# Optimization experiments

Measured on AMD Instinct MI355X. Metric: run time of the kernel, lower is better.

Reference implementation:

```python
import jax, jax.numpy as jnp
import numpy as np

B, N, DOP, DM, H = 8, 2048, 256, 256, 256  # batch, n_ops==n_machines, dims


def setup_inputs() -> dict:
    key = jax.random.key(0)
    ks = jax.random.split(key, 21)
    s = 0.02
    inp = {
        "operation_features": jax.random.normal(ks[0], (B, N, DOP), jnp.float32),
        "machine_features": jax.random.normal(ks[1], (B, N, DM), jnp.float32),
        "type_match_mask": jax.random.bernoulli(ks[2], 0.3, (B, N, N)).astype(jnp.float32),
        "same_type_mask": jax.random.bernoulli(ks[3], 0.3, (B, N, N)).astype(jnp.float32),
        "oma_q_w": jax.random.normal(ks[4], (H, DM), jnp.float32) * s,
        "oma_q_b": jnp.zeros((H,), jnp.float32),
        "oma_kv_w": jax.random.normal(ks[5], (2 * H, DOP), jnp.float32) * s,
        "oma_kv_b": jnp.zeros((2 * H,), jnp.float32),
        "oma_s_w": jax.random.normal(ks[6], (1, 2 * H), jnp.float32) * s,
        "oma_s_b": jnp.zeros((1,), jnp.float32),
        "oma_o_w": jax.random.normal(ks[7], (DM, H), jnp.float32) * s,
        "oma_o_b": jnp.zeros((DM,), jnp.float32),
        "sa_w_w": jax.random.normal(ks[8], (3 * H, DM), jnp.float32) * s,
        "sa_w_b": jnp.zeros((3 * H,), jnp.float32),
        "sa_s_w": jax.random.normal(ks[9], (1, 2 * H), jnp.float32) * s,
        "sa_s_b": jnp.zeros((1,), jnp.float32),
        "sa_o_w": jax.random.normal(ks[10], (DM, H), jnp.float32) * s,
        "sa_o_b": jnp.zeros((DM,), jnp.float32),
        "mix_w": jax.random.normal(ks[11], (DM, 2 * DM), jnp.float32) * s,
        "mix_b": jnp.zeros((DM,), jnp.float32),
    }
    return inp


def reference(operation_features, machine_features, type_match_mask, same_type_mask,
              oma_q_w, oma_q_b, oma_kv_w, oma_kv_b, oma_s_w, oma_s_b, oma_o_w, oma_o_b,
              sa_w_w, sa_w_b, sa_s_w, sa_s_b, sa_o_w, sa_o_b, mix_w, mix_b):
    # --- OperationMachineAttention ---
    q = machine_features @ oma_q_w.T + oma_q_b            # (B,M,H)
    kv = operation_features @ oma_kv_w.T + oma_kv_b       # (B,C,2H)
    k, v = jnp.split(kv, 2, axis=-1)
    # Linear(cat([q,k])) == q @ W[:, :H].T + k @ W[:, H:].T + b (additive-score factorization)
    sq = jnp.einsum('bmh,h->bm', q, oma_s_w[0, :H])
    sk = jnp.einsum('bch,h->bc', k, oma_s_w[0, H:])
    scores = jax.nn.leaky_relu(sq[:, :, None] + sk[:, None, :] + oma_s_b[0])  # (B,M,C)
    p = jax.nn.softmax(scores * type_match_mask, axis=-1)
    wf = jnp.einsum('bmc,bch->bmh', p, v)
    operation_machine = wf @ oma_o_w.T + oma_o_b           # (B,M,DM)

    # --- SelfAttention over machines ---
    w3 = machine_features @ sa_w_w.T + sa_w_b              # (B,C,3H)
    q2, k2, v2 = jnp.split(w3, 3, axis=-1)
    sq2 = jnp.einsum('bih,h->bi', q2, sa_s_w[0, :H])
    sk2 = jnp.einsum('bjh,h->bj', k2, sa_s_w[0, H:])
    s2 = jax.nn.leaky_relu(sq2[:, :, None] + sk2[:, None, :] + sa_s_b[0])  # (B,C,C)
    p2 = jax.nn.softmax(s2 * same_type_mask, axis=-1)
    machine_machine = jnp.einsum('bij,bjh->bih', p2, v2) @ sa_o_w.T + sa_o_b  # (B,C,DM)

    # --- mix ---
    mixed = jnp.concatenate([operation_machine, machine_machine], axis=-1)
    return mixed @ mix_w.T + mix_b                          # (B,N,DM)
```

## Files before the change

kernel.cpp:

```cpp
#include <hip/hip_runtime.h>
#include <stdint.h>
#include <stddef.h>

#define B_ 8
#define N_ 2048
#define C_ 2048
#define D_ 256
#define H_ 256

typedef __bf16 bf16x8 __attribute__((ext_vector_type(8)));
typedef __bf16 bf16x4 __attribute__((ext_vector_type(4)));
typedef float f32x4 __attribute__((ext_vector_type(4)));

#define MFMA16(a, b, c) __builtin_amdgcn_mfma_f32_16x16x32_bf16((a), (b), (c), 0, 0, 0)

__global__ __launch_bounds__(256) void k0_vectors(
    const float* __restrict__ oma_q_w, const float* __restrict__ oma_q_b,
    const float* __restrict__ oma_kv_w, const float* __restrict__ oma_kv_b,
    const float* __restrict__ oma_s_w, const float* __restrict__ oma_s_b,
    const float* __restrict__ sa_w_w, const float* __restrict__ sa_w_b,
    const float* __restrict__ sa_s_w, const float* __restrict__ sa_s_b,
    float* __restrict__ wq_v, float* __restrict__ wk_v,
    float* __restrict__ wq2_v, float* __restrict__ wk2_v,
    float* __restrict__ sb)
{
    int d = threadIdx.x;
    float a0 = 0.f, a1 = 0.f, a2 = 0.f, a3 = 0.f;
    for (int h = 0; h < 256; ++h) {
        a0 += oma_q_w[h * 256 + d] * oma_s_w[h];
        a1 += oma_kv_w[h * 256 + d] * oma_s_w[256 + h];
        a2 += sa_w_w[h * 256 + d] * sa_s_w[h];
        a3 += sa_w_w[(256 + h) * 256 + d] * sa_s_w[256 + h];
    }
    wq_v[d] = a0; wk_v[d] = a1; wq2_v[d] = a2; wk2_v[d] = a3;

    int h = d;
    float p1 = oma_q_b[h] * oma_s_w[h] + oma_kv_b[h] * oma_s_w[256 + h];
    float p2 = sa_w_b[h] * sa_s_w[h] + sa_w_b[256 + h] * sa_s_w[256 + h];
    for (int o = 32; o; o >>= 1) { p1 += __shfl_xor(p1, o); p2 += __shfl_xor(p2, o); }
    __shared__ float redA[4], redB[4];
    int wv = threadIdx.x >> 6;
    if ((threadIdx.x & 63) == 0) { redA[wv] = p1; redB[wv] = p2; }
    __syncthreads();
    if (threadIdx.x == 0) {
        sb[0] = redA[0] + redA[1] + redA[2] + redA[3] + oma_s_b[0];
        sb[1] = redB[0] + redB[1] + redB[2] + redB[3] + sa_s_b[0];
    }
}

__global__ __launch_bounds__(256) void k1_wcat(
    const float* __restrict__ mix_w, const float* __restrict__ mix_b,
    const float* __restrict__ oma_o_w, const float* __restrict__ oma_o_b,
    const float* __restrict__ sa_o_w, const float* __restrict__ sa_o_b,
    __bf16* __restrict__ Wcat, float* __restrict__ b_total)
{
    int d = blockIdx.x, h = threadIdx.x;
    const float* mwr = mix_w + d * 512;
    float w1 = 0.f, w2 = 0.f;
    for (int e = 0; e < 256; ++e) {
        w1 += mwr[e] * oma_o_w[e * 256 + h];
        w2 += mwr[256 + e] * sa_o_w[e * 256 + h];
    }
    Wcat[d * 512 + h] = (__bf16)w1;
    Wcat[d * 512 + 256 + h] = (__bf16)w2;

    float pb = mwr[h] * oma_o_b[h] + mwr[256 + h] * sa_o_b[h];
    for (int o = 32; o; o >>= 1) pb += __shfl_xor(pb, o);
    __shared__ float red[4];
    if ((h & 63) == 0) red[h >> 6] = pb;
    __syncthreads();
    if (h == 0) b_total[d] = mix_b[d] + red[0] + red[1] + red[2] + red[3];
}

__global__ __launch_bounds__(256) void k2_scores(
    const float* __restrict__ op, const float* __restrict__ mach,
    const float* __restrict__ wq_v, const float* __restrict__ wk_v,
    const float* __restrict__ wq2_v, const float* __restrict__ wk2_v,
    const float* __restrict__ sb,
    float* __restrict__ sqp, float* __restrict__ skv,
    float* __restrict__ sq2p, float* __restrict__ sk2v)
{
    int t = threadIdx.x, lane = t & 63, wv = t >> 6;
    size_t n = (size_t)blockIdx.x * 4 + wv;
    const float4 mf = *(const float4*)(mach + n * 256 + lane * 4);
    const float4 of = *(const float4*)(op + n * 256 + lane * 4);
    const float4 q4 = *(const float4*)(wq_v + lane * 4);
    const float4 k4 = *(const float4*)(wk_v + lane * 4);
    const float4 q24 = *(const float4*)(wq2_v + lane * 4);
    const float4 k24 = *(const float4*)(wk2_v + lane * 4);
    float s1 = mf.x * q4.x + mf.y * q4.y + mf.z * q4.z + mf.w * q4.w;
    float s2 = of.x * k4.x + of.y * k4.y + of.z * k4.z + of.w * k4.w;
    float s3 = mf.x * q24.x + mf.y * q24.y + mf.z * q24.z + mf.w * q24.w;
    float s4 = mf.x * k24.x + mf.y * k24.y + mf.z * k24.z + mf.w * k24.w;
    for (int o = 32; o; o >>= 1) {
        s1 += __shfl_xor(s1, o); s2 += __shfl_xor(s2, o);
        s3 += __shfl_xor(s3, o); s4 += __shfl_xor(s4, o);
    }
    if (lane == 0) {
        sqp[n] = s1 + sb[0]; skv[n] = s2;
        sq2p[n] = s3 + sb[1]; sk2v[n] = s4;
    }
}

__global__ __launch_bounds__(256, 2) void k3_vgemm(
    const float* __restrict__ op, const float* __restrict__ mach,
    const float* __restrict__ oma_kv_w, const float* __restrict__ sa_w_w,
    __bf16* __restrict__ vt)
{
    __shared__ __attribute__((aligned(16))) __bf16 As[64][72];
    __shared__ __attribute__((aligned(16))) __bf16 Bs[64][72];
    int t = threadIdx.x;
    int bid = blockIdx.x;
    int which = bid >> 10;
    int r = bid & 1023;
    int b = r >> 7;
    int ht = (r >> 5) & 3;
    int ct = r & 31;

    const float* Aglob = (which ? (sa_w_w + 512 * 256) : (oma_kv_w + 256 * 256)) + ht * 64 * 256;
    const float* Bglob = (which ? mach : op) + ((size_t)b * N_ + ct * 64) * 256;

    int lane = t & 63, wv = t >> 6;
    int l15 = lane & 15, qo = (lane >> 4) * 8;
    int rr = t >> 4;
    int dd = (t & 15) * 4;

    f32x4 acc[4] = {};

    for (int d0 = 0; d0 < 256; d0 += 64) {
        #pragma unroll
        for (int p = 0; p < 4; ++p) {
            float4 av = *(const float4*)(Aglob + (size_t)(p * 16 + rr) * 256 + d0 + dd);
            float4 bv = *(const float4*)(Bglob + (size_t)(p * 16 + rr) * 256 + d0 + dd);
            bf16x4 a4, b4;
            a4[0] = (__bf16)av.x; a4[1] = (__bf16)av.y; a4[2] = (__bf16)av.z; a4[3] = (__bf16)av.w;
            b4[0] = (__bf16)bv.x; b4[1] = (__bf16)bv.y; b4[2] = (__bf16)bv.z; b4[3] = (__bf16)bv.w;
            *(bf16x4*)&As[p * 16 + rr][dd] = a4;
            *(bf16x4*)&Bs[p * 16 + rr][dd] = b4;
        }
        __syncthreads();
        #pragma unroll
        for (int kb = 0; kb < 2; ++kb) {
            bf16x8 bfr = *(const bf16x8*)&Bs[16 * wv + l15][kb * 32 + qo];
            #pragma unroll
            for (int rt = 0; rt < 4; ++rt) {
                bf16x8 afr = *(const bf16x8*)&As[16 * rt + l15][kb * 32 + qo];
                acc[rt] = MFMA16(afr, bfr, acc[rt]);
            }
        }
        __syncthreads();
    }
    #pragma unroll
    for (int rt = 0; rt < 4; ++rt)
        #pragma unroll
        for (int j = 0; j < 4; ++j)
            As[16 * rt + (lane >> 4) * 4 + j][16 * wv + l15] = (__bf16)acc[rt][j];
    __syncthreads();
    int hh = t >> 2, cb = (t & 3) * 16;
    __bf16* orow = vt + (((size_t)(which * 8 + b)) * 256 + ht * 64 + hh) * 2048 + ct * 64 + cb;
    *(bf16x8*)(orow) = *(const bf16x8*)&As[hh][cb];
    *(bf16x8*)(orow + 8) = *(const bf16x8*)&As[hh][cb + 8];
}

__global__ __launch_bounds__(256, 2) void k4_attn(
    const float* __restrict__ tmask, const float* __restrict__ smask,
    const float* __restrict__ sqp, const float* __restrict__ skv,
    const float* __restrict__ sq2p, const float* __restrict__ sk2v,
    const __bf16* __restrict__ vt,
    __bf16* __restrict__ wfcat)
{
    __shared__ __attribute__((aligned(16))) __bf16 eA[64][72];
    __shared__ __attribute__((aligned(16))) __bf16 vB[256][72];
    __shared__ float rowsum[64];

    int t = threadIdx.x;
    int bid = blockIdx.x;
    int which = bid >> 8;
    int r = bid & 255;
    int b = r >> 5;
    int m0 = (r & 31) * 64;

    const float* mask = (which ? smask : tmask) + ((size_t)b * N_ + m0) * C_;
    const float* sqrow = (which ? sq2p : sqp) + b * N_ + m0;
    const float* skrow = (which ? sk2v : skv) + b * N_;
    const __bf16* vbase = vt + ((size_t)(which * 8 + b)) * 256 * 2048;

    int lane = t & 63, wv = t >> 6;
    int l15 = lane & 15, qo = (lane >> 4) * 8;
    int mrow = t >> 2;
    int cqb = (t & 3) * 16;
    int vh = t >> 3;
    int vc = (t & 7) * 8;

    float sqv = sqrow[mrow];
    float psum = 0.f;
    f32x4 acc[4][4] = {};

    bf16x8 vv[8];
    float mk[16], skc[16];

    auto load_tiles = [&](int c0) {
        #pragma unroll
        for (int p = 0; p < 8; ++p)
            vv[p] = *(const bf16x8*)(vbase + (size_t)(p * 32 + vh) * 2048 + c0 + vc);
        #pragma unroll
        for (int i = 0; i < 4; ++i) {
            float4 m4 = *(const float4*)(mask + (size_t)mrow * C_ + c0 + cqb + i * 4);
            float4 s4 = *(const float4*)(skrow + c0 + cqb + i * 4);
            mk[4 * i + 0] = m4.x; mk[4 * i + 1] = m4.y; mk[4 * i + 2] = m4.z; mk[4 * i + 3] = m4.w;
            skc[4 * i + 0] = s4.x; skc[4 * i + 1] = s4.y; skc[4 * i + 2] = s4.z; skc[4 * i + 3] = s4.w;
        }
    };
    load_tiles(0);

    for (int c0 = 0; c0 < C_; c0 += 64) {
        #pragma unroll
        for (int p = 0; p < 8; ++p)
            *(bf16x8*)&vB[p * 32 + vh][vc] = vv[p];
        bf16x8 e0, e1;
        #pragma unroll
        for (int i = 0; i < 16; ++i) {
            float s = sqv + skc[i];
            s = s > 0.f ? s : 0.01f * s;
            float e = __expf(s * mk[i]);
            psum += e;
            if (i < 8) e0[i] = (__bf16)e; else e1[i - 8] = (__bf16)e;
        }
        *(bf16x8*)&eA[mrow][cqb] = e0;
        *(bf16x8*)&eA[mrow][cqb + 8] = e1;
        __syncthreads();
        int cn = c0 + 64; if (cn >= C_) cn = 0;
        load_tiles(cn);
        #pragma unroll
        for (int kb = 0; kb < 2; ++kb) {
            bf16x8 afr[4];
            #pragma unroll
            for (int rt = 0; rt < 4; ++rt)
                afr[rt] = *(const bf16x8*)&eA[16 * rt + l15][kb * 32 + qo];
            #pragma unroll
            for (int ctile = 0; ctile < 4; ++ctile) {
                bf16x8 bfr = *(const bf16x8*)&vB[64 * wv + 16 * ctile + l15][kb * 32 + qo];
                #pragma unroll
                for (int rt = 0; rt < 4; ++rt)
                    acc[rt][ctile] = MFMA16(afr[rt], bfr, acc[rt][ctile]);
            }
        }
        __syncthreads();
    }

    float rs = psum;
    rs += __shfl_xor(rs, 1);
    rs += __shfl_xor(rs, 2);
    if ((t & 3) == 0) rowsum[mrow] = rs;
    __syncthreads();

    __bf16* obuf = &vB[0][0];
    #pragma unroll
    for (int rt = 0; rt < 4; ++rt) {
        #pragma unroll
        for (int j = 0; j < 4; ++j) {
            int m = 16 * rt + (lane >> 4) * 4 + j;
            float inv = __builtin_amdgcn_rcpf(rowsum[m]);
            #pragma unroll
            for (int ctile = 0; ctile < 4; ++ctile)
                obuf[m * 264 + 64 * wv + 16 * ctile + l15] = (__bf16)(acc[rt][ctile][j] * inv);
        }
    }
    __syncthreads();
    int m = t >> 2, cb = (t & 3) * 64;
    __bf16* wrow = wfcat + ((size_t)(b * N_ + m0 + m)) * 512 + which * 256 + cb;
    #pragma unroll
    for (int k = 0; k < 8; ++k)
        *(bf16x8*)(wrow + k * 8) = *(const bf16x8*)&obuf[m * 264 + cb + k * 8];
}

__global__ __launch_bounds__(256, 2) void k5_out(
    const __bf16* __restrict__ wfcat, const __bf16* __restrict__ Wcat,
    const float* __restrict__ b_total, float* __restrict__ out)
{
    __shared__ __attribute__((aligned(16))) __bf16 As[64][72];
    __shared__ __attribute__((aligned(16))) __bf16 Bs[256][72];
    __shared__ float bias[256];
    int t = threadIdx.x;
    int n0 = blockIdx.x * 64;
    int lane = t & 63, wv = t >> 6, l15 = lane & 15, qo = (lane >> 4) * 8;
    bias[t] = b_total[t];
    int ar = t >> 3;
    int ac = (t & 7) * 8;
    f32x4 acc[4][4] = {};

    for (int k0 = 0; k0 < 512; k0 += 64) {
        #pragma unroll
        for (int p = 0; p < 2; ++p)
            *(bf16x8*)&As[p * 32 + ar][ac] =
                *(const bf16x8*)(wfcat + (size_t)(n0 + p * 32 + ar) * 512 + k0 + ac);
        #pragma unroll
        for (int p = 0; p < 8; ++p)
            *(bf16x8*)&Bs[p * 32 + ar][ac] =
                *(const bf16x8*)(Wcat + (size_t)(p * 32 + ar) * 512 + k0 + ac);
        __syncthreads();
        #pragma unroll
        for (int kb = 0; kb < 2; ++kb) {
            bf16x8 afr[4];
            #pragma unroll
            for (int rt = 0; rt < 4; ++rt)
                afr[rt] = *(const bf16x8*)&As[16 * rt + l15][kb * 32 + qo];
            #pragma unroll
            for (int ct = 0; ct < 4; ++ct) {
                bf16x8 bfr = *(const bf16x8*)&Bs[64 * wv + 16 * ct + l15][kb * 32 + qo];
                #pragma unroll
                for (int rt = 0; rt < 4; ++rt)
                    acc[rt][ct] = MFMA16(afr[rt], bfr, acc[rt][ct]);
            }
        }
        __syncthreads();
    }
    #pragma unroll
    for (int rt = 0; rt < 4; ++rt) {
        #pragma unroll
        for (int ct = 0; ct < 4; ++ct) {
            int d = 64 * wv + 16 * ct + l15;
            float bv = bias[d];
            #pragma unroll
            for (int j = 0; j < 4; ++j) {
                int m = 16 * rt + (lane >> 4) * 4 + j;
                out[(size_t)(n0 + m) * 256 + d] = acc[rt][ct][j] + bv;
            }
        }
    }
}

extern "C" void kernel_launch(void* const* d_in, const int* in_sizes, int n_in,
                              void* d_out, int out_size, void* d_ws, size_t ws_size,
                              hipStream_t stream)
{
    const float* op_feat  = (const float*)d_in[0];
    const float* mach_feat= (const float*)d_in[1];
    const float* tmask    = (const float*)d_in[2];
    const float* smask    = (const float*)d_in[3];
    const float* oma_q_w  = (const float*)d_in[4];
    const float* oma_q_b  = (const float*)d_in[5];
    const float* oma_kv_w = (const float*)d_in[6];
    const float* oma_kv_b = (const float*)d_in[7];
    const float* oma_s_w  = (const float*)d_in[8];
    const float* oma_s_b  = (const float*)d_in[9];
    const float* oma_o_w  = (const float*)d_in[10];
    const float* oma_o_b  = (const float*)d_in[11];
    const float* sa_w_w   = (const float*)d_in[12];
    const float* sa_w_b   = (const float*)d_in[13];
    const float* sa_s_w   = (const float*)d_in[14];
    const float* sa_s_b   = (const float*)d_in[15];
    const float* sa_o_w   = (const float*)d_in[16];
    const float* sa_o_b   = (const float*)d_in[17];
    const float* mix_w    = (const float*)d_in[18];
    const float* mix_b    = (const float*)d_in[19];

    char* ws = (char*)d_ws;
    float* wq_v   = (float*)(ws + 0);
    float* wk_v   = (float*)(ws + 1024);
    float* wq2_v  = (float*)(ws + 2048);
    float* wk2_v  = (float*)(ws + 3072);
    float* sb     = (float*)(ws + 4096);
    float* btot   = (float*)(ws + 4352);
    float* sqp    = (float*)(ws + 8192);
    float* skv    = (float*)(ws + 73728);
    float* sq2p   = (float*)(ws + 139264);
    float* sk2v   = (float*)(ws + 204800);
    __bf16* Wcat  = (__bf16*)(ws + 270336);
    __bf16* vt    = (__bf16*)(ws + 532480);
    __bf16* wfcat = (__bf16*)(ws + 17309696);
    float* outp   = (float*)d_out;

    k0_vectors<<<1, 256, 0, stream>>>(oma_q_w, oma_q_b, oma_kv_w, oma_kv_b,
                                      oma_s_w, oma_s_b, sa_w_w, sa_w_b,
                                      sa_s_w, sa_s_b, wq_v, wk_v, wq2_v, wk2_v, sb);
    k1_wcat<<<256, 256, 0, stream>>>(mix_w, mix_b, oma_o_w, oma_o_b,
                                     sa_o_w, sa_o_b, Wcat, btot);
    k2_scores<<<4096, 256, 0, stream>>>(op_feat, mach_feat, wq_v, wk_v, wq2_v, wk2_v,
                                        sb, sqp, skv, sq2p, sk2v);
    k3_vgemm<<<2048, 256, 0, stream>>>(op_feat, mach_feat, oma_kv_w, sa_w_w, vt);
    k4_attn<<<512, 256, 0, stream>>>(tmask, smask, sqp, skv, sq2p, sk2v, vt, wfcat);
    k5_out<<<256, 256, 0, stream>>>(wfcat, Wcat, btot, outp);
}
```

Baseline: 453.1 us.

## Restructure V-projection GEMM and shrink attention row tiles with swizzled LDS

Measured after the change: 560.7 us. +23.8%, slower.

```diff
diff --git a/kernel.cpp b/kernel.cpp
--- a/kernel.cpp
+++ b/kernel.cpp
@@ -107,41 +107,47 @@
     const float* __restrict__ oma_kv_w, const float* __restrict__ sa_w_w,
     __bf16* __restrict__ vt)
 {
-    __shared__ __attribute__((aligned(16))) __bf16 As[64][72];
-    __shared__ __attribute__((aligned(16))) __bf16 Bs[64][72];
+    __shared__ __attribute__((aligned(16))) __bf16 Xs[64][264];
+    __shared__ __attribute__((aligned(16))) __bf16 As[64][264];
     int t = threadIdx.x;
     int bid = blockIdx.x;
-    int which = bid >> 10;
-    int r = bid & 1023;
-    int b = r >> 7;
-    int ht = (r >> 5) & 3;
+    int which = bid >> 8;
+    int r = bid & 255;
+    int b = r >> 5;
     int ct = r & 31;
 
-    const float* Aglob = (which ? (sa_w_w + 512 * 256) : (oma_kv_w + 256 * 256)) + ht * 64 * 256;
-    const float* Bglob = (which ? mach : op) + ((size_t)b * N_ + ct * 64) * 256;
+    const float* Wbase = which ? (sa_w_w + 512 * 256) : (oma_kv_w + 256 * 256);
+    const float* Xglob = (which ? mach : op) + ((size_t)b * N_ + ct * 64) * 256;
 
     int lane = t & 63, wv = t >> 6;
     int l15 = lane & 15, qo = (lane >> 4) * 8;
-    int rr = t >> 4;
-    int dd = (t & 15) * 4;
-
-    f32x4 acc[4] = {};
-
-    for (int d0 = 0; d0 < 256; d0 += 64) {
-        #pragma unroll
-        for (int p = 0; p < 4; ++p) {
-            float4 av = *(const float4*)(Aglob + (size_t)(p * 16 + rr) * 256 + d0 + dd);
-            float4 bv = *(const float4*)(Bglob + (size_t)(p * 16 + rr) * 256 + d0 + dd);
-            bf16x4 a4, b4;
+
+    #pragma unroll
+    for (int p = 0; p < 16; ++p) {
+        int row = p * 4 + wv;
+        float4 xv = *(const float4*)(Xglob + (size_t)row * 256 + lane * 4);
+        bf16x4 x4;
+        x4[0] = (__bf16)xv.x; x4[1] = (__bf16)xv.y; x4[2] = (__bf16)xv.z; x4[3] = (__bf16)xv.w;
+        *(bf16x4*)&Xs[row][lane * 4] = x4;
+    }
+
+    for (int ht = 0; ht < 4; ++ht) {
+        __syncthreads();
+        const float* Ag = Wbase + (size_t)ht * 64 * 256;
+        #pragma unroll
+        for (int p = 0; p < 16; ++p) {
+            int row = p * 4 + wv;
+            float4 av = *(const float4*)(Ag + (size_t)row * 256 + lane * 4);
+            bf16x4 a4;
             a4[0] = (__bf16)av.x; a4[1] = (__bf16)av.y; a4[2] = (__bf16)av.z; a4[3] = (__bf16)av.w;
-            b4[0] = (__bf16)bv.x; b4[1] = (__bf16)bv.y; b4[2] = (__bf16)bv.z; b4[3] = (__bf16)bv.w;
-            *(bf16x4*)&As[p * 16 + rr][dd] = a4;
-            *(bf16x4*)&Bs[p * 16 + rr][dd] = b4;
-        }
-        __syncthreads();
-        #pragma unroll
-        for (int kb = 0; kb < 2; ++kb) {
-            bf16x8 bfr = *(const bf16x8*)&Bs[16 * wv + l15][kb * 32 + qo];
+            *(bf16x4*)&As[row][lane * 4] = a4;
+        }
+        __syncthreads();
+
+        f32x4 acc[4] = {};
+        #pragma unroll
+        for (int kb = 0; kb < 8; ++kb) {
+            bf16x8 bfr = *(const bf16x8*)&Xs[16 * wv + l15][kb * 32 + qo];
             #pragma unroll
             for (int rt = 0; rt < 4; ++rt) {
                 bf16x8 afr = *(const bf16x8*)&As[16 * rt + l15][kb * 32 + qo];
@@ -149,36 +155,37 @@
             }
         }
         __syncthreads();
-    }
-    #pragma unroll
-    for (int rt = 0; rt < 4; ++rt)
-        #pragma unroll
-        for (int j = 0; j < 4; ++j)
-            As[16 * rt + (lane >> 4) * 4 + j][16 * wv + l15] = (__bf16)acc[rt][j];
-    __syncthreads();
-    int hh = t >> 2, cb = (t & 3) * 16;
-    __bf16* orow = vt + (((size_t)(which * 8 + b)) * 256 + ht * 64 + hh) * 2048 + ct * 64 + cb;
-    *(bf16x8*)(orow) = *(const bf16x8*)&As[hh][cb];
-    *(bf16x8*)(orow + 8) = *(const bf16x8*)&As[hh][cb + 8];
-}
-
-__global__ __launch_bounds__(256, 2) void k4_attn(
+
+        #pragma unroll
+        for (int rt = 0; rt < 4; ++rt)
+            #pragma unroll
+            for (int j = 0; j < 4; ++j)
+                As[16 * rt + (lane >> 4) * 4 + j][16 * wv + l15] = (__bf16)acc[rt][j];
+        __syncthreads();
+
+        int hh = t >> 2, cb = (t & 3) * 16;
+        __bf16* orow = vt + (((size_t)(which * 8 + b)) * 256 + ht * 64 + hh) * 2048 + ct * 64 + cb;
+        *(bf16x8*)(orow) = *(const bf16x8*)&As[hh][cb];
+        *(bf16x8*)(orow + 8) = *(const bf16x8*)&As[hh][cb + 8];
+    }
+}
+
+__global__ __launch_bounds__(256, 4) void k4_attn(
     const float* __restrict__ tmask, const float* __restrict__ smask,
     const float* __restrict__ sqp, const float* __restrict__ skv,
     const float* __restrict__ sq2p, const float* __restrict__ sk2v,
     const __bf16* __restrict__ vt,
     __bf16* __restrict__ wfcat)
 {
-    __shared__ __attribute__((aligned(16))) __bf16 eA[64][72];
+    __shared__ __attribute__((aligned(16))) __bf16 eA[32][64];
     __shared__ __attribute__((aligned(16))) __bf16 vB[256][72];
-    __shared__ float rowsum[64];
 
     int t = threadIdx.x;
     int bid = blockIdx.x;
-    int which = bid >> 8;
-    int r = bid & 255;
-    int b = r >> 5;
-    int m0 = (r & 31) * 64;
+    int which = bid >> 9;
+    int r = bid & 511;
+    int b = r >> 6;
+    int m0 = (r & 63) * 32;
 
     const float* mask = (which ? smask : tmask) + ((size_t)b * N_ + m0) * C_;
     const float* sqrow = (which ? sq2p : sqp) + b * N_ + m0;
@@ -187,76 +194,85 @@
 
     int lane = t & 63, wv = t >> 6;
     int l15 = lane & 15, qo = (lane >> 4) * 8;
-    int mrow = t >> 2;
-    int cqb = (t & 3) * 16;
+    int mrow = t >> 3;
+    int cc = t & 7;
     int vh = t >> 3;
     int vc = (t & 7) * 8;
 
     float sqv = sqrow[mrow];
     float psum = 0.f;
-    f32x4 acc[4][4] = {};
+    f32x4 acc[2][4] = {};
 
     bf16x8 vv[8];
-    float mk[16], skc[16];
-
-    auto load_tiles = [&](int c0) {
+    float mk[2][8], skc[2][8];
+
+    auto load_mask = [&](int c0, int s) {
+        #pragma unroll
+        for (int i = 0; i < 2; ++i) {
+            float4 m4 = *(const float4*)(mask + (size_t)mrow * C_ + c0 + cc * 8 + i * 4);
+            float4 s4 = *(const float4*)(skrow + c0 + cc * 8 + i * 4);
+            mk[s][4 * i + 0] = m4.x; mk[s][4 * i + 1] = m4.y;
+            mk[s][4 * i + 2] = m4.z; mk[s][4 * i + 3] = m4.w;
+            skc[s][4 * i + 0] = s4.x; skc[s][4 * i + 1] = s4.y;
+            skc[s][4 * i + 2] = s4.z; skc[s][4 * i + 3] = s4.w;
+        }
+    };
+    auto load_v = [&](int c0) {
         #pragma unroll
         for (int p = 0; p < 8; ++p)
             vv[p] = *(const bf16x8*)(vbase + (size_t)(p * 32 + vh) * 2048 + c0 + vc);
-        #pragma unroll
-        for (int i = 0; i < 4; ++i) {
-            float4 m4 = *(const float4*)(mask + (size_t)mrow * C_ + c0 + cqb + i * 4);
-            float4 s4 = *(const float4*)(skrow + c0 + cqb + i * 4);
-            mk[4 * i + 0] = m4.x; mk[4 * i + 1] = m4.y; mk[4 * i + 2] = m4.z; mk[4 * i + 3] = m4.w;
-            skc[4 * i + 0] = s4.x; skc[4 * i + 1] = s4.y; skc[4 * i + 2] = s4.z; skc[4 * i + 3] = s4.w;
-        }
     };
-    load_tiles(0);
+
+    load_mask(0, 0);
+    load_v(0);
+    load_mask(64, 1);
 
     for (int c0 = 0; c0 < C_; c0 += 64) {
+        int s = (c0 >> 6) & 1;
         #pragma unroll
         for (int p = 0; p < 8; ++p)
             *(bf16x8*)&vB[p * 32 + vh][vc] = vv[p];
-        bf16x8 e0, e1;
-        #pragma unroll
-        for (int i = 0; i < 16; ++i) {
-            float s = sqv + skc[i];
-            s = s > 0.f ? s : 0.01f * s;
-            float e = __expf(s * mk[i]);
+        bf16x8 e0;
+        #pragma unroll
+        for (int i = 0; i < 8; ++i) {
+            float sc = sqv + skc[s][i];
+            sc = sc > 0.f ? sc : 0.01f * sc;
+            float e = __expf(sc * mk[s][i]);
             psum += e;
-            if (i < 8) e0[i] = (__bf16)e; else e1[i - 8] = (__bf16)e;
-        }
-        *(bf16x8*)&eA[mrow][cqb] = e0;
-        *(bf16x8*)&eA[mrow][cqb + 8] = e1;
-        __syncthreads();
-        int cn = c0 + 64; if (cn >= C_) cn = 0;
-        load_tiles(cn);
+            e0[i] = (__bf16)e;
+        }
+        *(bf16x8*)&eA[mrow][(cc ^ (mrow & 7)) * 8] = e0;
+        __syncthreads();
+        load_v((c0 + 64) & 2047);
+        load_mask((c0 + 128) & 2047, s);
         #pragma unroll
         for (int kb = 0; kb < 2; ++kb) {
-            bf16x8 afr[4];
-            #pragma unroll
-            for (int rt = 0; rt < 4; ++rt)
-                afr[rt] = *(const bf16x8*)&eA[16 * rt + l15][kb * 32 + qo];
+            bf16x8 afr[2];
+            #pragma unroll
+            for (int rt = 0; rt < 2; ++rt)
+                afr[rt] = *(const bf16x8*)&eA[16 * rt + l15][((kb * 4 + (lane >> 4)) ^ (l15 & 7)) * 8];
             #pragma unroll
             for (int ctile = 0; ctile < 4; ++ctile) {
                 bf16x8 bfr = *(const bf16x8*)&vB[64 * wv + 16 * ctile + l15][kb * 32 + qo];
                 #pragma unroll
-                for (int rt = 0; rt < 4; ++rt)
+                for (int rt = 0; rt < 2; ++rt)
                     acc[rt][ctile] = MFMA16(afr[rt], bfr, acc[rt][ctile]);
             }
         }
         __syncthreads();
     }
 
+    float* rowsum = (float*)(&vB[0][0] + 9000);
     float rs = psum;
     rs += __shfl_xor(rs, 1);
     rs += __shfl_xor(rs, 2);
-    if ((t & 3) == 0) rowsum[mrow] = rs;
+    rs += __shfl_xor(rs, 4);
+    if ((t & 7) == 0) rowsum[mrow] = rs;
     __syncthreads();
 
     __bf16* obuf = &vB[0][0];
     #pragma unroll
-    for (int rt = 0; rt < 4; ++rt) {
+    for (int rt = 0; rt < 2; ++rt) {
         #pragma unroll
         for (int j = 0; j < 4; ++j) {
             int m = 16 * rt + (lane >> 4) * 4 + j;
@@ -267,10 +283,10 @@
         }
     }
     __syncthreads();
-    int m = t >> 2, cb = (t & 3) * 64;
+    int m = t >> 3, cb = (t & 7) * 32;
     __bf16* wrow = wfcat + ((size_t)(b * N_ + m0 + m)) * 512 + which * 256 + cb;
     #pragma unroll
-    for (int k = 0; k < 8; ++k)
+    for (int k = 0; k < 4; ++k)
         *(bf16x8*)(wrow + k * 8) = *(const bf16x8*)&obuf[m * 264 + cb + k * 8];
 }
 
@@ -378,7 +394,7 @@
                                      sa_o_w, sa_o_b, Wcat, btot);
     k2_scores<<<4096, 256, 0, stream>>>(op_feat, mach_feat, wq_v, wk_v, wq2_v, wk2_v,
                                         sb, sqp, skv, sq2p, sk2v);
-    k3_vgemm<<<2048, 256, 0, stream>>>(op_feat, mach_feat, oma_kv_w, sa_w_w, vt);
-    k4_attn<<<512, 256, 0, stream>>>(tmask, smask, sqp, skv, sq2p, sk2v, vt, wfcat);
+    k3_vgemm<<<512, 256, 0, stream>>>(op_feat, mach_feat, oma_kv_w, sa_w_w, vt);
+    k4_attn<<<1024, 256, 0, stream>>>(tmask, smask, sqp, skv, sq2p, sk2v, vt, wfcat);
     k5_out<<<256, 256, 0, stream>>>(wfcat, Wcat, btot, outp);
 }
```
